# Performance work log

Measured on AMD Instinct MI355X. Metric: run time of the kernel, lower is better.

## Reference

```python
import jax, jax.numpy as jnp
import numpy as np

H = W = 64      # input_resolution
WS = 8          # window_size
SS = 4          # shift_size
DIM = 96
HEADS = 4
HEAD_DIM = DIM // HEADS
SCALE = HEAD_DIM ** -0.5
N = WS * WS     # tokens per window
EPS = 1e-5


def _rel_pos_index():
    # static (N, N) int index into the (2*WS-1)^2 bias table
    coords = np.stack(np.meshgrid(np.arange(WS), np.arange(WS), indexing='ij'))  # (2, WS, WS)
    cf = coords.reshape(2, -1)                       # (2, N)
    rel = (cf[:, :, None] - cf[:, None, :]).transpose(1, 2, 0)  # (N, N, 2)
    rel[:, :, 0] += WS - 1
    rel[:, :, 1] += WS - 1
    rel[:, :, 0] *= 2 * WS - 1
    return rel.sum(-1)                               # (N, N)


def _attn_mask():
    # static (nW, N, N) 0/-100 mask for shifted windows
    img = np.zeros((H, W))
    cnt = 0
    sl = (slice(0, -WS), slice(-WS, -SS), slice(-SS, None))
    for hs in sl:
        for ws_ in sl:
            img[hs, ws_] = cnt
            cnt += 1
    mw = img.reshape(H // WS, WS, W // WS, WS).transpose(0, 2, 1, 3).reshape(-1, N)
    diff = mw[:, None, :] - mw[:, :, None]
    return np.where(diff != 0, -100.0, 0.0).astype(np.float32)


_RPI = jnp.asarray(_rel_pos_index())
_MASK = jnp.asarray(_attn_mask())  # (nW, N, N)


def _layernorm(x, g, b):
    mu = jnp.mean(x, axis=-1, keepdims=True)
    var = jnp.mean(jnp.square(x - mu), axis=-1, keepdims=True)
    return (x - mu) * jax.lax.rsqrt(var + EPS) * g + b


def setup_inputs() -> dict:
    key = jax.random.key(0)
    ks = jax.random.split(key, 8)
    s = 0.02
    return {
        'x': jax.random.normal(ks[0], (64, H * W, DIM), jnp.float32),
        'norm1_g': jnp.ones((DIM,), jnp.float32),
        'norm1_b': jnp.zeros((DIM,), jnp.float32),
        'qkv_w': jax.random.normal(ks[1], (3 * DIM, DIM), jnp.float32) * s,
        'qkv_b': jnp.zeros((3 * DIM,), jnp.float32),
        'rel_bias_table': jax.random.normal(ks[2], ((2 * WS - 1) ** 2, HEADS), jnp.float32) * s,
        'proj_w': jax.random.normal(ks[3], (DIM, DIM), jnp.float32) * s,
        'proj_b': jnp.zeros((DIM,), jnp.float32),
        'norm2_g': jnp.ones((DIM,), jnp.float32),
        'norm2_b': jnp.zeros((DIM,), jnp.float32),
        'fc1_w': jax.random.normal(ks[4], (4 * DIM, DIM), jnp.float32) * s,
        'fc1_b': jnp.zeros((4 * DIM,), jnp.float32),
        'fc2_w': jax.random.normal(ks[5], (DIM, 4 * DIM), jnp.float32) * s,
        'fc2_b': jnp.zeros((DIM,), jnp.float32),
    }


def reference(x, norm1_g, norm1_b, qkv_w, qkv_b, rel_bias_table, proj_w, proj_b,
              norm2_g, norm2_b, fc1_w, fc1_b, fc2_w, fc2_b):
    B, L, C = x.shape
    nW = (H // WS) * (W // WS)
    shortcut = x

    h = _layernorm(x, norm1_g, norm1_b).reshape(B, H, W, C)
    h = jnp.roll(h, (-SS, -SS), axis=(1, 2))
    # window partition -> (B*nW, N, C)
    h = h.reshape(B, H // WS, WS, W // WS, WS, C).transpose(0, 1, 3, 2, 4, 5)
    h = h.reshape(B * nW, N, C)

    qkv = h @ qkv_w.T + qkv_b                                   # (B_, N, 3C)
    qkv = qkv.reshape(B * nW, N, 3, HEADS, HEAD_DIM).transpose(2, 0, 3, 1, 4)
    q, k, v = qkv[0] * SCALE, qkv[1], qkv[2]                    # (B_, heads, N, hd)

    attn = jnp.einsum('whnd,whmd->whnm', q, k)                  # (B_, heads, N, N)
    bias = rel_bias_table[_RPI.reshape(-1)].reshape(N, N, HEADS).transpose(2, 0, 1)
    attn = attn + bias[None]
    attn = attn.reshape(B, nW, HEADS, N, N) + _MASK[None, :, None]
    attn = jax.nn.softmax(attn.reshape(B * nW, HEADS, N, N), axis=-1)

    out = jnp.einsum('whnm,whmd->whnd', attn, v)                # (B_, heads, N, hd)
    out = out.transpose(0, 2, 1, 3).reshape(B * nW, N, C)
    out = out @ proj_w.T + proj_b

    # window reverse + un-shift
    out = out.reshape(B, H // WS, W // WS, WS, WS, C).transpose(0, 1, 3, 2, 4, 5)
    out = out.reshape(B, H, W, C)
    out = jnp.roll(out, (SS, SS), axis=(1, 2)).reshape(B, L, C)

    x = shortcut + out
    h2 = _layernorm(x, norm2_g, norm2_b)
    h2 = jax.nn.gelu(h2 @ fc1_w.T + fc1_b, approximate=False)
    h2 = h2 @ fc2_w.T + fc2_b
    return x + h2
```

## Files before the change

### kernel.cpp

```cpp
#include <hip/hip_runtime.h>
#include <hip/hip_fp16.h>
#include <math.h>

typedef _Float16 half_t;
typedef _Float16 half8 __attribute__((ext_vector_type(8)));
typedef float f32x4 __attribute__((ext_vector_type(4)));

#define MFMA(a, b, c) __builtin_amdgcn_mfma_f32_16x16x32_f16((a), (b), (c), 0, 0, 0)
#define BARRIER() asm volatile("s_waitcnt lgkmcnt(0)\n\ts_barrier" ::: "memory")

static constexpr float kScale = 0.2041241452319315f;
static constexpr int RS   = 104;
static constexpr int QSTR = 200;
static constexpr int VTS  = 72;
static constexpr int H1S  = 392;

struct W3 { half8 b0, b1, b2; float bias; };

__device__ __forceinline__ W3 ld_w3(const half_t* w, const float* bv, int n0, int qo) {
  W3 r;
  const half_t* wp = w + (size_t)n0 * 96 + qo;
  r.b0 = *(const half8*)(wp);
  r.b1 = *(const half8*)(wp + 32);
  r.b2 = *(const half8*)(wp + 64);
  r.bias = bv[n0];
  return r;
}

__device__ __forceinline__ void qkv_tile(const W3& w, int t, int l15, int quad,
                                         const half8 (&af)[4][3],
                                         half_t* qbuf, half_t* vT) {
  f32x4 acc[4] = {{0,0,0,0},{0,0,0,0},{0,0,0,0},{0,0,0,0}};
#pragma unroll
  for (int g = 0; g < 4; ++g) acc[g] = MFMA(af[g][0], w.b0, acc[g]);
#pragma unroll
  for (int g = 0; g < 4; ++g) acc[g] = MFMA(af[g][1], w.b1, acc[g]);
#pragma unroll
  for (int g = 0; g < 4; ++g) acc[g] = MFMA(af[g][2], w.b2, acc[g]);
  int n0 = t * 16 + l15;
  if (t < 12) {
    float sc_ = (t < 6) ? kScale : 1.f;
#pragma unroll
    for (int g = 0; g < 4; ++g)
#pragma unroll
      for (int r = 0; r < 4; ++r)
        qbuf[(g * 16 + quad * 4 + r) * QSTR + n0] = (half_t)((acc[g][r] + w.bias) * sc_);
  } else {
    int vc = n0 - 192;
    int hd = vc / 24, c = vc - hd * 24;
#pragma unroll
    for (int g = 0; g < 4; ++g)
#pragma unroll
      for (int r = 0; r < 4; ++r)
        vT[hd * 24 * VTS + c * VTS + g * 16 + quad * 4 + r] = (half_t)(acc[g][r] + w.bias);
  }
}

__device__ __forceinline__ void fc1_tile(const W3& w, int t, int l15, int quad,
                                         const half8 (&a5)[2][3], half_t* h1h) {
  f32x4 a0 = {0,0,0,0}, a1 = {0,0,0,0};
  a0 = MFMA(a5[0][0], w.b0, a0); a1 = MFMA(a5[1][0], w.b0, a1);
  a0 = MFMA(a5[0][1], w.b1, a0); a1 = MFMA(a5[1][1], w.b1, a1);
  a0 = MFMA(a5[0][2], w.b2, a0); a1 = MFMA(a5[1][2], w.b2, a1);
  int n0 = t * 16 + l15;
#pragma unroll
  for (int g2 = 0; g2 < 2; ++g2) {
    const f32x4& ac = g2 ? a1 : a0;
#pragma unroll
    for (int r = 0; r < 4; ++r) {
      float vvv = ac[r] + w.bias;
      float u = vvv * (1.5957691216f + 0.1427096322f * vvv * vvv);
      float g = vvv * __builtin_amdgcn_rcpf(1.f + __expf(-u));
      h1h[(g2 * 16 + quad * 4 + r) * H1S + n0] = (half_t)g;
    }
  }
}

__device__ __forceinline__ void fc2_ld(const half_t* fc2w, int t, int l15, int qo,
                                       half8 (&bf)[12]) {
#pragma unroll
  for (int kt = 0; kt < 12; ++kt)
    bf[kt] = *(const half8*)(fc2w + (size_t)(t * 16 + l15) * 384 + kt * 32 + qo);
}

__device__ __forceinline__ void fc2_tile(const half8 (&a2)[12], const half8 (&bf)[12],
                                         int t, int hb, int rt, int l15, int quad,
                                         int wh, int ww, int bb,
                                         const float* fc2b, const half_t* rbuf,
                                         float* out) {
  f32x4 acc = {0,0,0,0};
#pragma unroll
  for (int kt = 0; kt < 12; ++kt) acc = MFMA(a2[kt], bf[kt], acc);
  int col = t * 16 + l15;
  float bias = fc2b[col];
#pragma unroll
  for (int r = 0; r < 4; ++r) {
    int tok = hb * 32 + rt * 16 + quad * 4 + r;
    int sr = (wh * 8 + (tok >> 3) + 4) & 63;
    int sc = (ww * 8 + (tok & 7) + 4) & 63;
    out[((size_t)bb * 4096 + sr * 64 + sc) * 96 + col] = (float)rbuf[tok * RS + col] + acc[r] + bias;
  }
}

__device__ __forceinline__ void p5_pass(int hb, int wave, int l15, int quad, int qo, int chh,
                                        const half_t* xn, half_t* h1h,
                                        const half_t* fc1w, const float* fc1b,
                                        const half_t* fc2w,
                                        W3& f1A, W3& f1B, half8 (&bfA)[12]) {
  half8 a5[2][3];
#pragma unroll
  for (int g2 = 0; g2 < 2; ++g2)
#pragma unroll
    for (int kt = 0; kt < 3; ++kt)
      a5[g2][kt] = *(const half8*)(&xn[((hb * 2 + g2) * 16 + l15) * RS + kt * 32 + quad * 8]);
  W3 f1C = ld_w3(fc1w, fc1b, (wave + 8) * 16 + l15, qo);
  fc1_tile(f1A, wave, l15, quad, a5, h1h);
  f1A = ld_w3(fc1w, fc1b, (wave + 12) * 16 + l15, qo);
  fc1_tile(f1B, wave + 4, l15, quad, a5, h1h);
  f1B = ld_w3(fc1w, fc1b, (wave + 16) * 16 + l15, qo);
  fc1_tile(f1C, wave + 8, l15, quad, a5, h1h);
  f1C = ld_w3(fc1w, fc1b, (wave + 20) * 16 + l15, qo);
  fc1_tile(f1A, wave + 12, l15, quad, a5, h1h);
  fc2_ld(fc2w, chh * 3 + 0, l15, qo, bfA);
  fc1_tile(f1B, wave + 16, l15, quad, a5, h1h);
  fc1_tile(f1C, wave + 20, l15, quad, a5, h1h);
}

__device__ __forceinline__ void p6_pass(int hb, int wave, int l15, int quad, int qo, int chh,
                                        int wh, int ww, int bb, bool pre_fc1,
                                        const half_t* h1h, const half_t* rbuf,
                                        const half_t* fc2w, const float* fc2b,
                                        const half_t* fc1w, const float* fc1b,
                                        float* out,
                                        W3& f1A, W3& f1B, half8 (&bfA)[12], half8 (&bfB)[12]) {
  int rt = wave >> 1;
  half8 a2[12];
#pragma unroll
  for (int kt = 0; kt < 12; ++kt)
    a2[kt] = *(const half8*)(&h1h[(rt * 16 + l15) * H1S + kt * 32 + quad * 8]);
  fc2_ld(fc2w, chh * 3 + 1, l15, qo, bfB);
  fc2_tile(a2, bfA, chh * 3 + 0, hb, rt, l15, quad, wh, ww, bb, fc2b, rbuf, out);
  fc2_ld(fc2w, chh * 3 + 2, l15, qo, bfA);
  fc2_tile(a2, bfB, chh * 3 + 1, hb, rt, l15, quad, wh, ww, bb, fc2b, rbuf, out);
  if (pre_fc1) {
    f1A = ld_w3(fc1w, fc1b, wave * 16 + l15, qo);
    f1B = ld_w3(fc1w, fc1b, (wave + 4) * 16 + l15, qo);
  }
  fc2_tile(a2, bfA, chh * 3 + 2, hb, rt, l15, quad, wh, ww, bb, fc2b, rbuf, out);
}

__global__ __launch_bounds__(256) void k_convert(const float* __restrict__ qkv_w,
                                                 const float* __restrict__ proj_w,
                                                 const float* __restrict__ fc1_w,
                                                 const float* __restrict__ fc2_w,
                                                 const float* __restrict__ tbl,
                                                 half_t* __restrict__ wbuf,
                                                 float* __restrict__ biasT) {
  int i = blockIdx.x * 256 + threadIdx.x;
  if (i < 27648)        wbuf[i] = (half_t)qkv_w[i];
  else if (i < 36864)   wbuf[i] = (half_t)proj_w[i - 27648];
  else if (i < 73728)   wbuf[i] = (half_t)fc1_w[i - 36864];
  else if (i < 110592)  wbuf[i] = (half_t)fc2_w[i - 73728];
  else if (biasT != nullptr) {
    int j = i - 110592;
    int h = j >> 12, rem = j & 4095;
    int ii = rem >> 6, jj = rem & 63;
    int ih = ii >> 3, iw = ii & 7, jh = jj >> 3, jw = jj & 7;
    biasT[j] = tbl[((ih - jh + 7) * 15 + (iw - jw + 7)) * 4 + h];
  }
}

__global__ __launch_bounds__(256, 3) void k_swin(
    const float* __restrict__ x,
    const float* __restrict__ n1g, const float* __restrict__ n1b,
    const half_t* __restrict__ qkvw, const float* __restrict__ qkv_b,
    const float* __restrict__ tbl_g, const float* __restrict__ biasT,
    const half_t* __restrict__ projw, const float* __restrict__ proj_b,
    const float* __restrict__ n2g, const float* __restrict__ n2b,
    const half_t* __restrict__ fc1w, const float* __restrict__ fc1b,
    const half_t* __restrict__ fc2w, const float* __restrict__ fc2b,
    float* __restrict__ out) {
  __shared__ __attribute__((aligned(16))) unsigned char smem[52736];
  half_t* qbuf = (half_t*)smem;
  half_t* h1h  = (half_t*)smem;
  half_t* vT   = (half_t*)(smem + 25600);
  half_t* rbuf = (half_t*)(smem + 25600);
  half_t* hn   = (half_t*)(smem + 39424);
  half_t* xn   = (half_t*)(smem + 39424);

  int tid = threadIdx.x;
  int wave = tid >> 6, lane = tid & 63;
  int l15 = lane & 15, quad = lane >> 4;
  int qo = quad * 8, chh = wave & 1;
  int blk = blockIdx.x;
  int bb = blk >> 6, wh = (blk >> 3) & 7, ww = blk & 7;

  float v[24];
  {
    int tok = wave * 16 + l15;
    int sr = (wh * 8 + (tok >> 3) + 4) & 63;
    int sc = (ww * 8 + (tok & 7) + 4) & 63;
    const float* rp = x + ((size_t)bb * 4096 + sr * 64 + sc) * 96;
#pragma unroll
    for (int kt = 0; kt < 3; ++kt) {
      float4 a = *(const float4*)(rp + kt * 32 + qo);
      float4 b = *(const float4*)(rp + kt * 32 + qo + 4);
      v[kt*8+0]=a.x; v[kt*8+1]=a.y; v[kt*8+2]=a.z; v[kt*8+3]=a.w;
      v[kt*8+4]=b.x; v[kt*8+5]=b.y; v[kt*8+6]=b.z; v[kt*8+7]=b.w;
    }
  }
  W3 qA = ld_w3(qkvw, qkv_b, wave * 16 + l15, qo);
  W3 qB = ld_w3(qkvw, qkv_b, (wave + 4) * 16 + l15, qo);
  {
    int tok = wave * 16 + l15;
    float s1 = 0.f, s2 = 0.f;
#pragma unroll
    for (int c = 0; c < 24; ++c) { s1 += v[c]; s2 += v[c] * v[c]; }
    s1 += __shfl_xor(s1, 16); s1 += __shfl_xor(s1, 32);
    s2 += __shfl_xor(s2, 16); s2 += __shfl_xor(s2, 32);
    float mu = s1 * (1.f / 96.f);
    float inv = rsqrtf(fmaxf(s2 * (1.f / 96.f) - mu * mu, 0.f) + 1e-5f);
#pragma unroll
    for (int kt = 0; kt < 3; ++kt) {
      int c0 = kt * 32 + qo;
      float4 g0 = *(const float4*)(n1g + c0);
      float4 g1 = *(const float4*)(n1g + c0 + 4);
      float4 b0 = *(const float4*)(n1b + c0);
      float4 b1 = *(const float4*)(n1b + c0 + 4);
      float gg[8] = {g0.x,g0.y,g0.z,g0.w,g1.x,g1.y,g1.z,g1.w};
      float bv[8] = {b0.x,b0.y,b0.z,b0.w,b1.x,b1.y,b1.z,b1.w};
      half8 hh;
#pragma unroll
      for (int j = 0; j < 8; ++j)
        hh[j] = (half_t)((v[kt*8+j] - mu) * inv * gg[j] + bv[j]);
      *(half8*)(&hn[tok * RS + kt * 32 + qo]) = hh;
    }
  }
  BARRIER();

  {
    W3 qC = ld_w3(qkvw, qkv_b, (wave + 8) * 16 + l15, qo);
    half8 af[4][3];
#pragma unroll
    for (int g = 0; g < 4; ++g)
#pragma unroll
      for (int kt = 0; kt < 3; ++kt)
        af[g][kt] = *(const half8*)(&hn[(g * 16 + l15) * RS + kt * 32 + qo]);
    qkv_tile(qA, wave, l15, quad, af, qbuf, vT);
    qA = ld_w3(qkvw, qkv_b, (wave + 12) * 16 + l15, qo);
    qkv_tile(qB, wave + 4, l15, quad, af, qbuf, vT);
    if (wave < 2) qB = ld_w3(qkvw, qkv_b, (wave + 16) * 16 + l15, qo);
    qkv_tile(qC, wave + 8, l15, quad, af, qbuf, vT);
    qkv_tile(qA, wave + 12, l15, quad, af, qbuf, vT);
    if (wave < 2) qkv_tile(qB, wave + 16, l15, quad, af, qbuf, vT);
  }
  int head = wave;
  float bt[4][16];
  if (biasT != nullptr) {
#pragma unroll
    for (int g2 = 0; g2 < 4; ++g2)
#pragma unroll
      for (int r = 0; r < 4; ++r) {
        const float* bp = biasT + (head << 12) + ((g2 * 16 + quad * 4 + r) << 6) + l15;
#pragma unroll
        for (int nt = 0; nt < 4; ++nt) bt[g2][r * 4 + nt] = bp[nt * 16];
      }
  }
  BARRIER();

  {
    const half8 z8 = {};
    half8 kb[4], vb[2][2];
#pragma unroll
    for (int nt = 0; nt < 4; ++nt) {
      half8 t = *(const half8*)(&qbuf[(nt * 16 + l15) * QSTR + 96 + head * 24 + qo]);
      kb[nt] = (quad < 3) ? t : z8;
    }
#pragma unroll
    for (int nt = 0; nt < 2; ++nt)
#pragma unroll
      for (int kt = 0; kt < 2; ++kt)
        vb[nt][kt] = *(const half8*)(&vT[head * 24 * VTS + (nt * 16 + l15) * VTS + kt * 32 + qo]);

    int rj[4], jh_[4], jw_[4];
#pragma unroll
    for (int nt = 0; nt < 4; ++nt) {
      int j = nt * 16 + l15;
      jh_[nt] = j >> 3; jw_[nt] = j & 7;
      int rr = wh * 8 + jh_[nt], cc = ww * 8 + jw_[nt];
      rj[nt] = ((rr < 56) ? 0 : ((rr < 60) ? 1 : 2)) * 3 + ((cc < 56) ? 0 : ((cc < 60) ? 1 : 2));
    }

    half_t* pb = vT + head * 24 * VTS;
    f32x4 oacc[4][2];

#pragma unroll
    for (int g2 = 0; g2 < 4; ++g2) {
      half8 qt = *(const half8*)(&qbuf[(g2 * 16 + l15) * QSTR + head * 24 + qo]);
      half8 qa = (quad < 3) ? qt : z8;
      f32x4 sv[4];
#pragma unroll
      for (int nt = 0; nt < 4; ++nt) {
        f32x4 a = {0, 0, 0, 0};
        sv[nt] = MFMA(qa, kb[nt], a);
      }
      float pinv[4];
#pragma unroll
      for (int r = 0; r < 4; ++r) {
        int i = g2 * 16 + quad * 4 + r;
        int ih = i >> 3, iw = i & 7;
        int rr = wh * 8 + ih, cc = ww * 8 + iw;
        int ri = ((rr < 56) ? 0 : ((rr < 60) ? 1 : 2)) * 3 + ((cc < 56) ? 0 : ((cc < 60) ? 1 : 2));
#pragma unroll
        for (int nt = 0; nt < 4; ++nt) {
          float bvv;
          if (biasT != nullptr) bvv = bt[g2][r * 4 + nt];
          else bvv = tbl_g[((ih - jh_[nt] + 7) * 15 + (iw - jw_[nt] + 7)) * 4 + head];
          float val = sv[nt][r] + bvv;
          if (ri != rj[nt]) val -= 100.f;
          sv[nt][r] = val;
        }
        float mx = fmaxf(fmaxf(sv[0][r], sv[1][r]), fmaxf(sv[2][r], sv[3][r]));
        mx = fmaxf(mx, __shfl_xor(mx, 1));
        mx = fmaxf(mx, __shfl_xor(mx, 2));
        mx = fmaxf(mx, __shfl_xor(mx, 4));
        mx = fmaxf(mx, __shfl_xor(mx, 8));
        float sum = 0.f;
#pragma unroll
        for (int nt = 0; nt < 4; ++nt) {
          float e = __expf(sv[nt][r] - mx);
          sv[nt][r] = e;
          sum += e;
        }
        sum += __shfl_xor(sum, 1);
        sum += __shfl_xor(sum, 2);
        sum += __shfl_xor(sum, 4);
        sum += __shfl_xor(sum, 8);
        pinv[r] = __builtin_amdgcn_rcpf(sum);
      }
#pragma unroll
      for (int nt = 0; nt < 4; ++nt)
#pragma unroll
        for (int r = 0; r < 4; ++r)
          pb[(quad * 4 + r) * VTS + nt * 16 + l15] = (half_t)(sv[nt][r] * pinv[r]);
      __builtin_amdgcn_sched_barrier(0);
      half8 pa0 = *(const half8*)(&pb[l15 * VTS + qo]);
      half8 pa1 = *(const half8*)(&pb[l15 * VTS + 32 + qo]);
#pragma unroll
      for (int nt = 0; nt < 2; ++nt) {
        f32x4 a = {0, 0, 0, 0};
        a = MFMA(pa0, vb[nt][0], a);
        a = MFMA(pa1, vb[nt][1], a);
        oacc[g2][nt] = a;
      }
    }
#pragma unroll
    for (int g2 = 0; g2 < 4; ++g2)
#pragma unroll
      for (int nt = 0; nt < 2; ++nt) {
        int c = nt * 16 + l15;
        if (c < 24)
#pragma unroll
          for (int r = 0; r < 4; ++r)
            qbuf[(g2 * 16 + quad * 4 + r) * QSTR + head * 24 + c] = (half_t)oacc[g2][nt][r];
      }
  }
  W3 pw[6];
#pragma unroll
  for (int t = 0; t < 6; ++t) pw[t] = ld_w3(projw, proj_b, t * 16 + l15, qo);
  float xv[6][4];
#pragma unroll
  for (int r = 0; r < 4; ++r) {
    int tok2 = wave * 16 + quad * 4 + r;
    int sr = (wh * 8 + (tok2 >> 3) + 4) & 63;
    int sc = (ww * 8 + (tok2 & 7) + 4) & 63;
    const float* xp = x + ((size_t)bb * 4096 + sr * 64 + sc) * 96 + l15;
#pragma unroll
    for (int t = 0; t < 6; ++t) xv[t][r] = xp[t * 16];
  }
  float gn2[6], bn2[6];
#pragma unroll
  for (int t = 0; t < 6; ++t) { gn2[t] = n2g[t * 16 + l15]; bn2[t] = n2b[t * 16 + l15]; }
  BARRIER();

  {
    half8 oa[3];
#pragma unroll
    for (int kt = 0; kt < 3; ++kt)
      oa[kt] = *(const half8*)(&qbuf[(wave * 16 + l15) * QSTR + kt * 32 + qo]);
    f32x4 acc[6];
#pragma unroll
    for (int t = 0; t < 6; ++t) {
      f32x4 a = {0, 0, 0, 0};
      a = MFMA(oa[0], pw[t].b0, a);
      a = MFMA(oa[1], pw[t].b1, a);
      a = MFMA(oa[2], pw[t].b2, a);
      acc[t] = a;
    }
    float rv[6][4];
    float s1[4] = {0, 0, 0, 0}, s2[4] = {0, 0, 0, 0};
#pragma unroll
    for (int t = 0; t < 6; ++t)
#pragma unroll
      for (int r = 0; r < 4; ++r) {
        float vvv = xv[t][r] + acc[t][r] + pw[t].bias;
        rv[t][r] = vvv;
        s1[r] += vvv; s2[r] += vvv * vvv;
      }
    float mu[4], nv[4];
#pragma unroll
    for (int r = 0; r < 4; ++r) {
      s1[r] += __shfl_xor(s1[r], 1); s1[r] += __shfl_xor(s1[r], 2);
      s1[r] += __shfl_xor(s1[r], 4); s1[r] += __shfl_xor(s1[r], 8);
      s2[r] += __shfl_xor(s2[r], 1); s2[r] += __shfl_xor(s2[r], 2);
      s2[r] += __shfl_xor(s2[r], 4); s2[r] += __shfl_xor(s2[r], 8);
      mu[r] = s1[r] * (1.f / 96.f);
      nv[r] = rsqrtf(fmaxf(s2[r] * (1.f / 96.f) - mu[r] * mu[r], 0.f) + 1e-5f);
    }
#pragma unroll
    for (int t = 0; t < 6; ++t) {
      int n0 = t * 16 + l15;
#pragma unroll
      for (int r = 0; r < 4; ++r) {
        int row = wave * 16 + quad * 4 + r;
        rbuf[row * RS + n0] = (half_t)rv[t][r];
        xn[row * RS + n0] = (half_t)((rv[t][r] - mu[r]) * nv[r] * gn2[t] + bn2[t]);
      }
    }
  }
  W3 f1A = ld_w3(fc1w, fc1b, wave * 16 + l15, qo);
  W3 f1B = ld_w3(fc1w, fc1b, (wave + 4) * 16 + l15, qo);
  half8 bfA[12], bfB[12];
  BARRIER();

  p5_pass(0, wave, l15, quad, qo, chh, xn, h1h, fc1w, fc1b, fc2w, f1A, f1B, bfA);
  BARRIER();
  p6_pass(0, wave, l15, quad, qo, chh, wh, ww, bb, true,
          h1h, rbuf, fc2w, fc2b, fc1w, fc1b, out, f1A, f1B, bfA, bfB);
  BARRIER();
  p5_pass(1, wave, l15, quad, qo, chh, xn, h1h, fc1w, fc1b, fc2w, f1A, f1B, bfA);
  BARRIER();
  p6_pass(1, wave, l15, quad, qo, chh, wh, ww, bb, false,
          h1h, rbuf, fc2w, fc2b, fc1w, fc1b, out, f1A, f1B, bfA, bfB);
}

extern "C" void kernel_launch(void* const* d_in, const int* in_sizes, int n_in,
                              void* d_out, int out_size, void* d_ws, size_t ws_size,
                              hipStream_t stream) {
  const float* x      = (const float*)d_in[0];
  const float* n1g    = (const float*)d_in[1];
  const float* n1b    = (const float*)d_in[2];
  const float* qkv_w  = (const float*)d_in[3];
  const float* qkv_b  = (const float*)d_in[4];
  const float* rtbl   = (const float*)d_in[5];
  const float* proj_w = (const float*)d_in[6];
  const float* proj_b = (const float*)d_in[7];
  const float* n2g    = (const float*)d_in[8];
  const float* n2b    = (const float*)d_in[9];
  const float* fc1_w  = (const float*)d_in[10];
  const float* fc1_b  = (const float*)d_in[11];
  const float* fc2_w  = (const float*)d_in[12];
  const float* fc2_b  = (const float*)d_in[13];
  float* out = (float*)d_out;

  if (ws_size < 221184) return;
  half_t* wbuf = (half_t*)d_ws;
  float* biasT = (ws_size >= 221184 + 65536) ? (float*)((char*)d_ws + 221184) : nullptr;

  k_convert<<<496, 256, 0, stream>>>(qkv_w, proj_w, fc1_w, fc2_w, rtbl, wbuf, biasT);
  k_swin<<<4096, 256, 0, stream>>>(x, n1g, n1b, wbuf, qkv_b, rtbl, biasT,
                                   wbuf + 27648, proj_b, n2g, n2b,
                                   wbuf + 36864, fc1_b, wbuf + 73728, fc2_b, out);
}
```

Measured before the change: 406.8 us.

## Shrink shared memory by aliasing buffers to raise occupancy to four blocks per CU

Shared memory drops from 52736 to 40960 bytes by aliasing hn/qbuf/rbuf and xn/h1h into overlapping regions. To make the aliasing safe, LN1 and LN2 activations are loaded into registers up front (af, a5b), with extra barriers before the buffers get overwritten. Launch bounds rise from 3 to 4 blocks per CU, and the fc1 weight prefetch moves into a templated p5_pass. This targets higher occupancy to hide latency, at the cost of more register pressure, since all 4x3 fragments are held live under a tighter register budget, which could cause spills.

```diff
diff --git a/kernel.cpp b/kernel.cpp
--- a/kernel.cpp
+++ b/kernel.cpp
@@ -57,11 +57,12 @@
 }
 
 __device__ __forceinline__ void fc1_tile(const W3& w, int t, int l15, int quad,
-                                         const half8 (&a5)[2][3], half_t* h1h) {
+                                         const half8 (&a0f)[3], const half8 (&a1f)[3],
+                                         half_t* h1h) {
   f32x4 a0 = {0,0,0,0}, a1 = {0,0,0,0};
-  a0 = MFMA(a5[0][0], w.b0, a0); a1 = MFMA(a5[1][0], w.b0, a1);
-  a0 = MFMA(a5[0][1], w.b1, a0); a1 = MFMA(a5[1][1], w.b1, a1);
-  a0 = MFMA(a5[0][2], w.b2, a0); a1 = MFMA(a5[1][2], w.b2, a1);
+  a0 = MFMA(a0f[0], w.b0, a0); a1 = MFMA(a1f[0], w.b0, a1);
+  a0 = MFMA(a0f[1], w.b1, a0); a1 = MFMA(a1f[1], w.b1, a1);
+  a0 = MFMA(a0f[2], w.b2, a0); a1 = MFMA(a1f[2], w.b2, a1);
   int n0 = t * 16 + l15;
 #pragma unroll
   for (int g2 = 0; g2 < 2; ++g2) {
@@ -102,50 +103,43 @@
   }
 }
 
-__device__ __forceinline__ void p5_pass(int hb, int wave, int l15, int quad, int qo, int chh,
-                                        const half_t* xn, half_t* h1h,
+template <int BASE, bool LOADF1>
+__device__ __forceinline__ void p5_pass(const half8 (&a5b)[4][3], int wave, int l15,
+                                        int quad, int qo, int chh, half_t* h1h,
                                         const half_t* fc1w, const float* fc1b,
                                         const half_t* fc2w,
                                         W3& f1A, W3& f1B, half8 (&bfA)[12]) {
-  half8 a5[2][3];
-#pragma unroll
-  for (int g2 = 0; g2 < 2; ++g2)
-#pragma unroll
-    for (int kt = 0; kt < 3; ++kt)
-      a5[g2][kt] = *(const half8*)(&xn[((hb * 2 + g2) * 16 + l15) * RS + kt * 32 + quad * 8]);
-  W3 f1C = ld_w3(fc1w, fc1b, (wave + 8) * 16 + l15, qo);
-  fc1_tile(f1A, wave, l15, quad, a5, h1h);
-  f1A = ld_w3(fc1w, fc1b, (wave + 12) * 16 + l15, qo);
-  fc1_tile(f1B, wave + 4, l15, quad, a5, h1h);
-  f1B = ld_w3(fc1w, fc1b, (wave + 16) * 16 + l15, qo);
-  fc1_tile(f1C, wave + 8, l15, quad, a5, h1h);
-  f1C = ld_w3(fc1w, fc1b, (wave + 20) * 16 + l15, qo);
-  fc1_tile(f1A, wave + 12, l15, quad, a5, h1h);
+  if (LOADF1) {
+    f1A = ld_w3(fc1w, fc1b, wave * 16 + l15, qo);
+    f1B = ld_w3(fc1w, fc1b, (wave + 4) * 16 + l15, qo);
+  }
+  fc1_tile(f1A, wave, l15, quad, a5b[BASE], a5b[BASE + 1], h1h);
+  f1A = ld_w3(fc1w, fc1b, (wave + 8) * 16 + l15, qo);
+  fc1_tile(f1B, wave + 4, l15, quad, a5b[BASE], a5b[BASE + 1], h1h);
+  f1B = ld_w3(fc1w, fc1b, (wave + 12) * 16 + l15, qo);
+  fc1_tile(f1A, wave + 8, l15, quad, a5b[BASE], a5b[BASE + 1], h1h);
+  f1A = ld_w3(fc1w, fc1b, (wave + 16) * 16 + l15, qo);
+  fc1_tile(f1B, wave + 12, l15, quad, a5b[BASE], a5b[BASE + 1], h1h);
+  f1B = ld_w3(fc1w, fc1b, (wave + 20) * 16 + l15, qo);
+  fc1_tile(f1A, wave + 16, l15, quad, a5b[BASE], a5b[BASE + 1], h1h);
   fc2_ld(fc2w, chh * 3 + 0, l15, qo, bfA);
-  fc1_tile(f1B, wave + 16, l15, quad, a5, h1h);
-  fc1_tile(f1C, wave + 20, l15, quad, a5, h1h);
+  fc1_tile(f1B, wave + 20, l15, quad, a5b[BASE], a5b[BASE + 1], h1h);
 }
 
 __device__ __forceinline__ void p6_pass(int hb, int wave, int l15, int quad, int qo, int chh,
-                                        int wh, int ww, int bb, bool pre_fc1,
+                                        int wh, int ww, int bb,
                                         const half_t* h1h, const half_t* rbuf,
                                         const half_t* fc2w, const float* fc2b,
-                                        const half_t* fc1w, const float* fc1b,
-                                        float* out,
-                                        W3& f1A, W3& f1B, half8 (&bfA)[12], half8 (&bfB)[12]) {
+                                        float* out, half8 (&bfA)[12], half8 (&bfB)[12]) {
   int rt = wave >> 1;
   half8 a2[12];
 #pragma unroll
   for (int kt = 0; kt < 12; ++kt)
-    a2[kt] = *(const half8*)(&h1h[(rt * 16 + l15) * H1S + kt * 32 + quad * 8]);
+    a2[kt] = *(const half8*)(&h1h[(rt * 16 + l15) * H1S + kt * 32 + qo]);
   fc2_ld(fc2w, chh * 3 + 1, l15, qo, bfB);
   fc2_tile(a2, bfA, chh * 3 + 0, hb, rt, l15, quad, wh, ww, bb, fc2b, rbuf, out);
   fc2_ld(fc2w, chh * 3 + 2, l15, qo, bfA);
   fc2_tile(a2, bfB, chh * 3 + 1, hb, rt, l15, quad, wh, ww, bb, fc2b, rbuf, out);
-  if (pre_fc1) {
-    f1A = ld_w3(fc1w, fc1b, wave * 16 + l15, qo);
-    f1B = ld_w3(fc1w, fc1b, (wave + 4) * 16 + l15, qo);
-  }
   fc2_tile(a2, bfA, chh * 3 + 2, hb, rt, l15, quad, wh, ww, bb, fc2b, rbuf, out);
 }
 
@@ -170,7 +164,7 @@
   }
 }
 
-__global__ __launch_bounds__(256, 3) void k_swin(
+__global__ __launch_bounds__(256, 4) void k_swin(
     const float* __restrict__ x,
     const float* __restrict__ n1g, const float* __restrict__ n1b,
     const half_t* __restrict__ qkvw, const float* __restrict__ qkv_b,
@@ -180,13 +174,13 @@
     const half_t* __restrict__ fc1w, const float* __restrict__ fc1b,
     const half_t* __restrict__ fc2w, const float* __restrict__ fc2b,
     float* __restrict__ out) {
-  __shared__ __attribute__((aligned(16))) unsigned char smem[52736];
+  __shared__ __attribute__((aligned(16))) unsigned char smem[40960];
+  half_t* hn   = (half_t*)smem;
   half_t* qbuf = (half_t*)smem;
-  half_t* h1h  = (half_t*)smem;
   half_t* vT   = (half_t*)(smem + 25600);
-  half_t* rbuf = (half_t*)(smem + 25600);
-  half_t* hn   = (half_t*)(smem + 39424);
-  half_t* xn   = (half_t*)(smem + 39424);
+  half_t* rbuf = (half_t*)smem;
+  half_t* xn   = (half_t*)(smem + 13312);
+  half_t* h1h  = (half_t*)(smem + 13312);
 
   int tid = threadIdx.x;
   int wave = tid >> 6, lane = tid & 63;
@@ -238,14 +232,16 @@
   }
   BARRIER();
 
+  W3 qC = ld_w3(qkvw, qkv_b, (wave + 8) * 16 + l15, qo);
+  half8 af[4][3];
+#pragma unroll
+  for (int g = 0; g < 4; ++g)
+#pragma unroll
+    for (int kt = 0; kt < 3; ++kt)
+      af[g][kt] = *(const half8*)(&hn[(g * 16 + l15) * RS + kt * 32 + qo]);
+  BARRIER();
+
   {
-    W3 qC = ld_w3(qkvw, qkv_b, (wave + 8) * 16 + l15, qo);
-    half8 af[4][3];
-#pragma unroll
-    for (int g = 0; g < 4; ++g)
-#pragma unroll
-      for (int kt = 0; kt < 3; ++kt)
-        af[g][kt] = *(const half8*)(&hn[(g * 16 + l15) * RS + kt * 32 + qo]);
     qkv_tile(qA, wave, l15, quad, af, qbuf, vT);
     qA = ld_w3(qkvw, qkv_b, (wave + 12) * 16 + l15, qo);
     qkv_tile(qB, wave + 4, l15, quad, af, qbuf, vT);
@@ -388,6 +384,7 @@
 #pragma unroll
     for (int kt = 0; kt < 3; ++kt)
       oa[kt] = *(const half8*)(&qbuf[(wave * 16 + l15) * QSTR + kt * 32 + qo]);
+    BARRIER();
     f32x4 acc[6];
 #pragma unroll
     for (int t = 0; t < 6; ++t) {
@@ -433,15 +430,21 @@
   half8 bfA[12], bfB[12];
   BARRIER();
 
-  p5_pass(0, wave, l15, quad, qo, chh, xn, h1h, fc1w, fc1b, fc2w, f1A, f1B, bfA);
-  BARRIER();
-  p6_pass(0, wave, l15, quad, qo, chh, wh, ww, bb, true,
-          h1h, rbuf, fc2w, fc2b, fc1w, fc1b, out, f1A, f1B, bfA, bfB);
-  BARRIER();
-  p5_pass(1, wave, l15, quad, qo, chh, xn, h1h, fc1w, fc1b, fc2w, f1A, f1B, bfA);
-  BARRIER();
-  p6_pass(1, wave, l15, quad, qo, chh, wh, ww, bb, false,
-          h1h, rbuf, fc2w, fc2b, fc1w, fc1b, out, f1A, f1B, bfA, bfB);
+  half8 a5b[4][3];
+#pragma unroll
+  for (int g = 0; g < 4; ++g)
+#pragma unroll
+    for (int kt = 0; kt < 3; ++kt)
+      a5b[g][kt] = *(const half8*)(&xn[(g * 16 + l15) * RS + kt * 32 + qo]);
+  BARRIER();
+
+  p5_pass<0, false>(a5b, wave, l15, quad, qo, chh, h1h, fc1w, fc1b, fc2w, f1A, f1B, bfA);
+  BARRIER();
+  p6_pass(0, wave, l15, quad, qo, chh, wh, ww, bb, h1h, rbuf, fc2w, fc2b, out, bfA, bfB);
+  BARRIER();
+  p5_pass<2, true>(a5b, wave, l15, quad, qo, chh, h1h, fc1w, fc1b, fc2w, f1A, f1B, bfA);
+  BARRIER();
+  p6_pass(1, wave, l15, quad, qo, chh, wh, ww, bb, h1h, rbuf, fc2w, fc2b, out, bfA, bfB);
 }
 
 extern "C" void kernel_launch(void* const* d_in, const int* in_sizes, int n_in,
```

After: 496.5 us. 1.22x slower.
